# Optimization experiments

Hardware: AMD Instinct MI355X
Metric: run time of the kernel (lower is better)

The kernel has to match this reference:

```python
import jax, jax.numpy as jnp
import numpy as np

B, N1, N2, D, H, L, ITERS = 256, 64, 64, 256, 8, 18, 200
DH = D // H
LAYER_NAMES = ['self', 'cross'] * 9
OFFSET_MULT, NORMAL_MULT = 0.5, 10.0
FLIP = np.array([1.0, -1.0, -1.0], dtype=np.float32)


def setup_inputs() -> dict:
    key = jax.random.key(0)
    ks = jax.random.split(key, 16)
    s = 0.02
    inp = {
        'planeApp1': jax.random.normal(ks[0], (B, N1, D), jnp.float32),
        'planeApp2': jax.random.normal(ks[1], (B, N2, D), jnp.float32),
        'matcher_inputCam': jax.random.normal(ks[2], (B, 7), jnp.float32),
        'parameters1_local': jax.random.normal(ks[3], (B, N1, 3), jnp.float32),
        'parameters2_local': jax.random.normal(ks[4], (B, N2, 3), jnp.float32),
        'app_W': jax.random.normal(ks[5], (D, D), jnp.float32) * s,
        'app_b': jnp.zeros((D,), jnp.float32),
        'desc_W': jax.random.normal(ks[6], (D, D), jnp.float32) * s,
        'desc_b': jnp.zeros((D,), jnp.float32),
        'bin_score': jnp.asarray(1.0, jnp.float32),
        'gnn_Wq': jax.random.normal(ks[7], (L, D, D), jnp.float32) * s,
        'gnn_Wk': jax.random.normal(ks[8], (L, D, D), jnp.float32) * s,
        'gnn_Wv': jax.random.normal(ks[9], (L, D, D), jnp.float32) * s,
        'gnn_Wm': jax.random.normal(ks[10], (L, D, D), jnp.float32) * s,
        'gnn_W1': jax.random.normal(ks[11], (L, 2 * D, 2 * D), jnp.float32) * s,
        'gnn_W2': jax.random.normal(ks[12], (L, 2 * D, D), jnp.float32) * s,
        'gnn_ln1_g': jnp.ones((L, D), jnp.float32),
        'gnn_ln1_b': jnp.zeros((L, D), jnp.float32),
        'gnn_ln2_g': jnp.ones((L, D), jnp.float32),
        'gnn_ln2_b': jnp.zeros((L, D), jnp.float32),
    }
    return inp


def _layer_norm(x, g, b):
    m = jnp.mean(x, -1, keepdims=True)
    v = jnp.var(x, -1, keepdims=True)
    return (x - m) * jax.lax.rsqrt(v + 1e-5) * g + b


def _normalize(x):
    return x / jnp.clip(jnp.linalg.norm(x, axis=-1, keepdims=True), 1e-12)


def _quat_to_rot(q):
    q = q / jnp.linalg.norm(q, axis=-1, keepdims=True)
    w, x, y, z = q[:, 0], q[:, 1], q[:, 2], q[:, 3]
    R = jnp.stack([1 - 2 * (y * y + z * z), 2 * (x * y - w * z), 2 * (x * z + w * y),
                   2 * (x * y + w * z), 1 - 2 * (x * x + z * z), 2 * (y * z - w * x),
                   2 * (x * z - w * y), 2 * (y * z + w * x), 1 - 2 * (x * x + y * y)], axis=-1)
    return R.reshape(-1, 3, 3)


def _warp(plane, quat, tran):
    # plane [B,n,3], quat [B,4], tran [B,3] -> warped plane params [B,n,3]
    R = _quat_to_rot(quat)
    end = jnp.einsum('bij,bnj->bni', R, plane * FLIP) + tran[:, None, :]
    b = end - tran[:, None, :]
    scale = jnp.sum(end * b, -1) / (jnp.linalg.norm(b, axis=-1) + 1e-5) ** 2
    return scale[..., None] * b


def _lin_attn(q, k, v):
    # LoFTR linear attention; q [B,N,H,DH], k/v [B,M,H,DH]
    Q = jax.nn.elu(q) + 1.0
    K = jax.nn.elu(k) + 1.0
    v_len = v.shape[1]
    KV = jnp.einsum('bmhd,bmhe->bhde', K, v / v_len)
    Zden = 1.0 / (jnp.einsum('bnhd,bhd->bnh', Q, K.sum(1)) + 1e-6)
    return jnp.einsum('bnhd,bhde,bnh->bnhe', Q, KV, Zden) * v_len


def _enc_layer(x, src, Wq, Wk, Wv, Wm, W1, W2, g1, be1, g2, be2):
    Bx, N, _ = x.shape
    M = src.shape[1]
    q = (x @ Wq).reshape(Bx, N, H, DH)
    k = (src @ Wk).reshape(Bx, M, H, DH)
    v = (src @ Wv).reshape(Bx, M, H, DH)
    msg = _lin_attn(q, k, v).reshape(Bx, N, D)
    msg = _layer_norm(msg @ Wm, g1, be1)
    msg = _layer_norm(jax.nn.relu(jnp.concatenate([x, msg], -1) @ W1) @ W2, g2, be2)
    return x + msg


def reference(planeApp1, planeApp2, matcher_inputCam, parameters1_local, parameters2_local,
              app_W, app_b, desc_W, desc_b, bin_score,
              gnn_Wq, gnn_Wk, gnn_Wv, gnn_Wm, gnn_W1, gnn_W2,
              gnn_ln1_g, gnn_ln1_b, gnn_ln2_g, gnn_ln2_b):
    tran, quat = matcher_inputCam[:, :3], matcher_inputCam[:, 3:]
    # --- geometric priors (detached in the original) ---
    p2w = parameters2_local * FLIP  # warp with pose_n=1, no rot/tran
    offset2 = jnp.linalg.norm(p2w, axis=-1)  # [B,N2]
    normal2 = _normalize(p2w)
    p1_r = _warp(parameters1_local, quat, tran * 0.0)
    normal1_r = _normalize(p1_r)
    normal_dist = jnp.arccos(jnp.clip(jnp.einsum('bnd,bmd->bnm', normal1_r, normal2), -1.0, 1.0)) / np.pi * 180.0
    p1_rt = _warp(parameters1_local, quat, tran)
    offset1 = jnp.linalg.norm(p1_rt, axis=-1)  # [B,N1]
    normal1_rt = _normalize(p1_rt)
    nTn_rt = jnp.einsum('bnd,bmd->bnm', normal1_rt, normal2)
    od = jnp.where(nTn_rt < 0,
                   jnp.abs(offset1[:, :, None] + offset2[:, None, :]),
                   jnp.abs(offset1[:, :, None] - offset2[:, None, :]))
    offset_dist = jax.lax.stop_gradient(jnp.clip(od, 1e-10, 5.0))
    normal_dist = jax.lax.stop_gradient(normal_dist)
    # --- appearance projection (1x1 Conv1d == per-token linear) ---
    x0 = planeApp1 @ app_W + app_b
    x1 = planeApp2 @ app_W + app_b
    for i, name in enumerate(LAYER_NAMES):
        p = (gnn_Wq[i], gnn_Wk[i], gnn_Wv[i], gnn_Wm[i], gnn_W1[i], gnn_W2[i],
             gnn_ln1_g[i], gnn_ln1_b[i], gnn_ln2_g[i], gnn_ln2_b[i])
        if name == 'self':
            x0, x1 = _enc_layer(x0, x0, *p), _enc_layer(x1, x1, *p)
        else:
            x0, x1 = _enc_layer(x0, x1, *p), _enc_layer(x1, x0, *p)
    d1 = x0 @ desc_W + desc_b
    d2 = x1 @ desc_W + desc_b
    scores = jnp.einsum('bnd,bmd->bnm', d1, d2) / jnp.sqrt(jnp.float32(D))
    scores = scores - offset_dist / OFFSET_MULT - normal_dist / NORMAL_MULT
    # --- padded optimal transport (all rows/cols valid -> no -inf masking) ---
    pc = jnp.broadcast_to(bin_score, (B, N1, 1))
    pr = jnp.broadcast_to(bin_score, (B, 1, N2 + 1))
    Z = jnp.concatenate([jnp.concatenate([scores, pc], axis=2), pr], axis=1)  # [B,N1+1,N2+1]
    norm = -jnp.log(jnp.float32(N1 + N2))
    log_mu = jnp.broadcast_to(jnp.concatenate([jnp.full((N1,), norm), (jnp.log(jnp.float32(N2)) + norm)[None]]), (B, N1 + 1))
    log_nu = jnp.broadcast_to(jnp.concatenate([jnp.full((N2,), norm), (jnp.log(jnp.float32(N1)) + norm)[None]]), (B, N2 + 1))

    def step(carry, _):
        u, v = carry
        u = log_mu - jax.nn.logsumexp(Z + v[:, None, :], axis=2)
        v = log_nu - jax.nn.logsumexp(Z + u[:, :, None], axis=1)
        return (u, v), None

    (u, v), _ = jax.lax.scan(step, (jnp.zeros_like(log_mu), jnp.zeros_like(log_nu)), None, length=ITERS)
    return Z + u[:, :, None] + v[:, None, :] - norm
```

## Files before the change

kernel.cpp:

```cpp
#include <hip/hip_runtime.h>
#include <math.h>
#include <stddef.h>
#include <stdint.h>

typedef unsigned short u16;
typedef unsigned int   u32;

static constexpr int B_   = 256;
static constexpr int N_   = 64;
static constexpr int D_   = 256;
static constexpr int L_   = 18;
static constexpr int RM   = B_ * N_;
static constexpr int RM2  = 2 * RM;
static constexpr size_t SZb = (size_t)RM2 * D_;

typedef __attribute__((ext_vector_type(8))) short bf16x8;
typedef __attribute__((ext_vector_type(4))) float f32x4;

__device__ __forceinline__ float b2f(u16 u) {
    return __uint_as_float(((u32)u) << 16);
}
__device__ __forceinline__ u16 f2b(float f) {
    u32 x = __float_as_uint(f);
    return (u16)((x + 0x7FFFu + ((x >> 16) & 1u)) >> 16);
}
__device__ __forceinline__ void gl_lds16(const void* g, void* l) {
    __builtin_amdgcn_global_load_lds(
        (const __attribute__((address_space(1))) u32*)g,
        (__attribute__((address_space(3))) u32*)l, 16, 0, 0);
}

template<int K, int CONCAT, int RELU, int BIAS, int OUTF, int OUTB>
__global__ __launch_bounds__(256)
void mgemm(const u16* __restrict__ A1, const u16* __restrict__ A2,
           const u16* __restrict__ Bt, const float* __restrict__ bias,
           float* __restrict__ Cf, u16* __restrict__ Cb,
           int M, int splitn)
{
    constexpr int NT = K / 64;
    __shared__ u16 As[2][128 * 64];
    __shared__ u16 Bs[2][128 * 64];
    const int tid  = threadIdx.x;
    const int w    = tid >> 6;
    const int lane = tid & 63;
    const int wr   = w >> 1, wc = w & 1;
    const int row0 = blockIdx.x * 128;
    const int col0 = blockIdx.y * 128;
    const int lr   = lane & 15;
    const int lk   = (lane >> 4) * 8;
    const int srow = lane >> 3;
    const int schk = (lane & 7) * 8;

    auto stage = [&](int t, int buf) {
        const int k0 = t * 64;
        const u16* Aeff; int kloc, lda;
        if (CONCAT) {
            if (k0 < 256) { Aeff = A1; kloc = k0; } else { Aeff = A2; kloc = k0 - 256; }
            lda = 256;
        } else { Aeff = A1; kloc = k0; lda = K; }
        #pragma unroll
        for (int q = 0; q < 4; ++q) {
            const int i = w * 4 + q;
            gl_lds16(Aeff + (size_t)(row0 + i * 8 + srow) * lda + kloc + schk,
                     &As[buf][i * 512]);
            gl_lds16(Bt + (size_t)(col0 + i * 8 + srow) * K + t * 64 + schk,
                     &Bs[buf][i * 512]);
        }
    };

    f32x4 acc[4][4];
    #pragma unroll
    for (int m = 0; m < 4; ++m)
        #pragma unroll
        for (int n = 0; n < 4; ++n)
            acc[m][n] = (f32x4){0.f, 0.f, 0.f, 0.f};

    stage(0, 0);
    __syncthreads();
    #pragma unroll
    for (int t = 0; t < NT; ++t) {
        const int cur = t & 1;
        if (t + 1 < NT) stage(t + 1, cur ^ 1);
        #pragma unroll
        for (int kk = 0; kk < 2; ++kk) {
            bf16x8 af[4], bfr[4];
            #pragma unroll
            for (int m = 0; m < 4; ++m)
                af[m] = *(const bf16x8*)&As[cur][(wr * 64 + m * 16 + lr) * 64 + kk * 32 + lk];
            #pragma unroll
            for (int n = 0; n < 4; ++n)
                bfr[n] = *(const bf16x8*)&Bs[cur][(wc * 64 + n * 16 + lr) * 64 + kk * 32 + lk];
            #pragma unroll
            for (int m = 0; m < 4; ++m)
                #pragma unroll
                for (int n = 0; n < 4; ++n)
                    acc[m][n] = __builtin_amdgcn_mfma_f32_16x16x32_bf16(
                        af[m], bfr[n], acc[m][n], 0, 0, 0);
        }
        __syncthreads();
    }

    const size_t cbase = (size_t)(col0 / splitn) * (size_t)M * splitn;
    const int lc0 = col0 % splitn;
    #pragma unroll
    for (int m = 0; m < 4; ++m) {
        #pragma unroll
        for (int n = 0; n < 4; ++n) {
            const int gc = lc0 + wc * 64 + n * 16 + (lane & 15);
            #pragma unroll
            for (int r = 0; r < 4; ++r) {
                const int gr = row0 + wr * 64 + m * 16 + (lane >> 4) * 4 + r;
                float v = acc[m][n][r];
                if (BIAS) v += bias[gc];
                if (RELU) v = fmaxf(v, 0.f);
                const size_t idx = cbase + (size_t)gr * splitn + gc;
                if (OUTF) Cf[idx] = v;
                if (OUTB) Cb[idx] = f2b(v);
            }
        }
    }
}

template<int K, int RES>
__global__ __launch_bounds__(512)
void mgemm_ln(const u16* __restrict__ A, const u16* __restrict__ Bt,
              const float* __restrict__ g, const float* __restrict__ beta,
              const u16* __restrict__ resb, u16* __restrict__ outb)
{
    constexpr int NT = K / 64;
    __shared__ u16 As[2][128 * 64];
    __shared__ u16 Bs[2][256 * 64];
    __shared__ float rs[4][128], rq[4][128];
    const int tid  = threadIdx.x;
    const int w    = tid >> 6;
    const int lane = tid & 63;
    const int wr   = w >> 2, wc = w & 3;
    const int row0 = blockIdx.x * 128;
    const int lr   = lane & 15;
    const int lk   = (lane >> 4) * 8;
    const int srow = lane >> 3;
    const int schk = (lane & 7) * 8;

    auto stage = [&](int t, int buf) {
        #pragma unroll
        for (int q = 0; q < 2; ++q) {
            const int i = w * 2 + q;
            gl_lds16(A + (size_t)(row0 + i * 8 + srow) * K + t * 64 + schk,
                     &As[buf][i * 512]);
        }
        #pragma unroll
        for (int q = 0; q < 4; ++q) {
            const int i = w * 4 + q;
            gl_lds16(Bt + (size_t)(i * 8 + srow) * K + t * 64 + schk,
                     &Bs[buf][i * 512]);
        }
    };

    f32x4 acc[4][4];
    #pragma unroll
    for (int m = 0; m < 4; ++m)
        #pragma unroll
        for (int n = 0; n < 4; ++n)
            acc[m][n] = (f32x4){0.f, 0.f, 0.f, 0.f};

    stage(0, 0);
    __syncthreads();
    #pragma unroll
    for (int t = 0; t < NT; ++t) {
        const int cur = t & 1;
        if (t + 1 < NT) stage(t + 1, cur ^ 1);
        #pragma unroll
        for (int kk = 0; kk < 2; ++kk) {
            bf16x8 af[4], bfr[4];
            #pragma unroll
            for (int m = 0; m < 4; ++m)
                af[m] = *(const bf16x8*)&As[cur][(wr * 64 + m * 16 + lr) * 64 + kk * 32 + lk];
            #pragma unroll
            for (int n = 0; n < 4; ++n)
                bfr[n] = *(const bf16x8*)&Bs[cur][(wc * 64 + n * 16 + lr) * 64 + kk * 32 + lk];
            #pragma unroll
            for (int m = 0; m < 4; ++m)
                #pragma unroll
                for (int n = 0; n < 4; ++n)
                    acc[m][n] = __builtin_amdgcn_mfma_f32_16x16x32_bf16(
                        af[m], bfr[n], acc[m][n], 0, 0, 0);
        }
        __syncthreads();
    }

    #pragma unroll
    for (int m = 0; m < 4; ++m) {
        #pragma unroll
        for (int r = 0; r < 4; ++r) {
            float s  = acc[m][0][r] + acc[m][1][r] + acc[m][2][r] + acc[m][3][r];
            float s2 = acc[m][0][r]*acc[m][0][r] + acc[m][1][r]*acc[m][1][r]
                     + acc[m][2][r]*acc[m][2][r] + acc[m][3][r]*acc[m][3][r];
            #pragma unroll
            for (int o = 1; o < 16; o <<= 1) {
                s  += __shfl_xor(s,  o);
                s2 += __shfl_xor(s2, o);
            }
            if ((lane & 15) == 0) {
                const int row = wr * 64 + m * 16 + (lane >> 4) * 4 + r;
                rs[wc][row] = s; rq[wc][row] = s2;
            }
        }
    }
    __syncthreads();
    if (tid < 128) {
        const float s = rs[0][tid] + rs[1][tid] + rs[2][tid] + rs[3][tid];
        const float q = rq[0][tid] + rq[1][tid] + rq[2][tid] + rq[3][tid];
        const float mean = s * (1.f / 256.f);
        const float var  = q * (1.f / 256.f) - mean * mean;
        rs[0][tid] = mean;
        rq[0][tid] = rsqrtf(var + 1e-5f);
    }
    __syncthreads();

    float gc[4], bc[4];
    #pragma unroll
    for (int n = 0; n < 4; ++n) {
        const int col = wc * 64 + n * 16 + lr;
        gc[n] = g[col]; bc[n] = beta[col];
    }
    #pragma unroll
    for (int m = 0; m < 4; ++m) {
        #pragma unroll
        for (int r = 0; r < 4; ++r) {
            const int row  = wr * 64 + m * 16 + (lane >> 4) * 4 + r;
            const float mean = rs[0][row], inv = rq[0][row];
            const int gr = row0 + row;
            #pragma unroll
            for (int n = 0; n < 4; ++n) {
                const int col = wc * 64 + n * 16 + lr;
                const size_t idx = (size_t)gr * 256 + col;
                float y = (acc[m][n][r] - mean) * inv * gc[n] + bc[n];
                if (RES) y += b2f(resb[idx]);
                outb[idx] = f2b(y);
            }
        }
    }
}

__global__ __launch_bounds__(256)
void wtrans_kernel(const float* __restrict__ W, u16* __restrict__ Wt,
                   int K, int N, size_t in_lstride, size_t out_lstride,
                   int row_off, int ldk)
{
    __shared__ float T[64][65];
    const int k0 = blockIdx.x * 64, n0 = blockIdx.y * 64, l = blockIdx.z;
    const int t = threadIdx.x;
    const int r = t >> 2, c0 = (t & 3) * 16;
    const float* src = W + (size_t)l * in_lstride;
    #pragma unroll
    for (int q = 0; q < 4; ++q) {
        float4 v = *(const float4*)&src[(size_t)(k0 + r) * N + n0 + c0 + q * 4];
        T[r][c0 + q * 4 + 0] = v.x; T[r][c0 + q * 4 + 1] = v.y;
        T[r][c0 + q * 4 + 2] = v.z; T[r][c0 + q * 4 + 3] = v.w;
    }
    __syncthreads();
    u16 tmp[16];
    #pragma unroll
    for (int i = 0; i < 16; ++i) tmp[i] = f2b(T[c0 + i][r]);
    u16* dst = Wt + (size_t)l * out_lstride + (size_t)(row_off + n0 + r) * ldk + k0 + c0;
    *(uint4*)&dst[0] = *(const uint4*)&tmp[0];
    *(uint4*)&dst[8] = *(const uint4*)&tmp[8];
}

__global__ __launch_bounds__(256)
void cvt2_kernel(const float* __restrict__ s1, const float* __restrict__ s2,
                 u16* __restrict__ dst, int n4half)
{
    int i = blockIdx.x * 256 + threadIdx.x;
    if (i >= 2 * n4half) return;
    const float* s = (i < n4half) ? s1 : s2;
    const int ii = (i < n4half) ? i : i - n4half;
    float4 v = *(const float4*)&s[(size_t)ii * 4];
    u16 o[4] = {f2b(v.x), f2b(v.y), f2b(v.z), f2b(v.w)};
    *(uint2*)&dst[(size_t)i * 4] = *(const uint2*)&o[0];
}

__global__ __launch_bounds__(256)
void attn_kernel(const u16* __restrict__ Q, const u16* __restrict__ K,
                 const u16* __restrict__ V, u16* __restrict__ Mout, int selfl)
{
    const int bid = blockIdx.x;
    const int h = bid & 7;
    const int b = (bid >> 3) & 255;
    const int s = bid >> 11;
    const int ss = selfl ? s : (1 - s);
    const size_t qoff = ((size_t)(s  * RM) + b * N_) * D_ + h * 32;
    const size_t koff = ((size_t)(ss * RM) + b * N_) * D_ + h * 32;

    __shared__ float Ks[64][32];
    __shared__ float Vs[64][32];
    __shared__ float Qs[64][33];
    __shared__ float KV[32][32];
    __shared__ float Ksum[32];
    __shared__ float zden[64];

    const int t = threadIdx.x;
    {
        const int m = t >> 2, d0 = (t & 3) * 8;
        uint4 kq = *(const uint4*)&K[koff + (size_t)m * D_ + d0];
        uint4 vq = *(const uint4*)&V[koff + (size_t)m * D_ + d0];
        uint4 qq = *(const uint4*)&Q[qoff + (size_t)m * D_ + d0];
        const u16* kp = (const u16*)&kq;
        const u16* vp = (const u16*)&vq;
        const u16* qp = (const u16*)&qq;
        #pragma unroll
        for (int j = 0; j < 8; ++j) {
            float kx = b2f(kp[j]);
            Ks[m][d0 + j] = kx > 0.f ? kx + 1.f : __expf(kx);
            Vs[m][d0 + j] = b2f(vp[j]);
            float qx = b2f(qp[j]);
            Qs[m][d0 + j] = qx > 0.f ? qx + 1.f : __expf(qx);
        }
    }
    __syncthreads();
    if (t < 32) {
        float sacc = 0.f;
        for (int m = 0; m < 64; ++m) sacc += Ks[m][t];
        Ksum[t] = sacc;
    }
    for (int i = t; i < 32 * 32; i += 256) {
        const int d = i >> 5, e = i & 31;
        float acc = 0.f;
        for (int m = 0; m < 64; ++m) acc += Ks[m][d] * Vs[m][e];
        KV[d][e] = acc * (1.f / 64.f);
    }
    __syncthreads();
    if (t < 64) {
        float acc = 0.f;
        for (int d = 0; d < 32; ++d) acc += Qs[t][d] * Ksum[d];
        zden[t] = 1.f / (acc + 1e-6f);
    }
    __syncthreads();
    const int n = t >> 2, eg = t & 3;
    float acc[8] = {0.f,0.f,0.f,0.f,0.f,0.f,0.f,0.f};
    for (int d = 0; d < 32; ++d) {
        const float qv = Qs[n][d];
        #pragma unroll
        for (int j = 0; j < 8; ++j) acc[j] += qv * KV[d][eg * 8 + j];
    }
    const float zm = zden[n] * 64.f;
    u16 o[8];
    #pragma unroll
    for (int j = 0; j < 8; ++j) o[j] = f2b(acc[j] * zm);
    *(uint4*)&Mout[qoff + (size_t)n * D_ + eg * 8] = *(const uint4*)&o[0];
}

__global__ __launch_bounds__(64)
void geom_kernel(const float* __restrict__ cam, const float* __restrict__ p1,
                 const float* __restrict__ p2, float* __restrict__ pen)
{
    const int b = blockIdx.x;
    const int n = threadIdx.x;

    const float tx = cam[b*7+0], ty = cam[b*7+1], tz = cam[b*7+2];
    float qw = cam[b*7+3], qx = cam[b*7+4], qy = cam[b*7+5], qz = cam[b*7+6];
    const float qn = rsqrtf(qw*qw + qx*qx + qy*qy + qz*qz);
    qw *= qn; qx *= qn; qy *= qn; qz *= qn;
    const float r00 = 1.f - 2.f*(qy*qy + qz*qz), r01 = 2.f*(qx*qy - qw*qz), r02 = 2.f*(qx*qz + qw*qy);
    const float r10 = 2.f*(qx*qy + qw*qz), r11 = 1.f - 2.f*(qx*qx + qz*qz), r12 = 2.f*(qy*qz - qw*qx);
    const float r20 = 2.f*(qx*qz - qw*qy), r21 = 2.f*(qy*qz + qw*qx), r22 = 1.f - 2.f*(qx*qx + qy*qy);

    const float px =  p1[((size_t)b*64 + n)*3 + 0];
    const float py = -p1[((size_t)b*64 + n)*3 + 1];
    const float pz = -p1[((size_t)b*64 + n)*3 + 2];
    const float ex = r00*px + r01*py + r02*pz;
    const float ey = r10*px + r11*py + r12*pz;
    const float ez = r20*px + r21*py + r22*pz;
    const float el2 = ex*ex + ey*ey + ez*ez;
    const float el  = sqrtf(el2);
    float den = el + 1e-5f; den = den * den;
    const float sr  = el2 / den;
    const float prx = sr*ex, pry = sr*ey, prz = sr*ez;
    const float prl = fmaxf(sqrtf(prx*prx + pry*pry + prz*prz), 1e-12f);
    const float n1rx = prx/prl, n1ry = pry/prl, n1rz = prz/prl;
    const float dot_eb = (ex+tx)*ex + (ey+ty)*ey + (ez+tz)*ez;
    const float st  = dot_eb / den;
    const float ptx = st*ex, pty = st*ey, ptz = st*ez;
    const float o1  = sqrtf(ptx*ptx + pty*pty + ptz*ptz);
    const float ptl = fmaxf(o1, 1e-12f);
    const float n1tx = ptx/ptl, n1ty = pty/ptl, n1tz = ptz/ptl;
    const float ux =  p2[((size_t)b*64 + n)*3 + 0];
    const float uy = -p2[((size_t)b*64 + n)*3 + 1];
    const float uz = -p2[((size_t)b*64 + n)*3 + 2];
    const float o2 = sqrtf(ux*ux + uy*uy + uz*uz);
    const float ul = fmaxf(o2, 1e-12f);

    __shared__ float S[64][4];
    S[n][0] = ux/ul; S[n][1] = uy/ul; S[n][2] = uz/ul; S[n][3] = o2;
    __syncthreads();

    const float RAD2DEG = 57.295779513082323f;
    for (int m = 0; m < 64; ++m) {
        const float nx = S[m][0], ny = S[m][1], nz = S[m][2], o2m = S[m][3];
        float cosr = n1rx*nx + n1ry*ny + n1rz*nz;
        cosr = fminf(fmaxf(cosr, -1.f), 1.f);
        const float ndist = acosf(cosr) * RAD2DEG;
        const float cost = n1tx*nx + n1ty*ny + n1tz*nz;
        float od = (cost < 0.f) ? fabsf(o1 + o2m) : fabsf(o1 - o2m);
        od = fminf(fmaxf(od, 1e-10f), 5.f);
        pen[((size_t)b*64 + n)*64 + m] = od * 2.f + ndist * 0.1f;
    }
}

__global__ __launch_bounds__(256)
void zbuild_kernel(const float* __restrict__ dfeat, const float* __restrict__ pen,
                   const float* __restrict__ binp, float* __restrict__ Z)
{
    const int b = blockIdx.x;
    const float* d1 = dfeat + (size_t)(b * 64) * 256;
    const float* d2 = dfeat + (size_t)(RM + b * 64) * 256;
    __shared__ float D1[64][65], D2[64][65];
    const int tid = threadIdx.x;
    const int txx = tid & 15, tyy = tid >> 4;
    float acc[4][4] = {{0.f,0.f,0.f,0.f},{0.f,0.f,0.f,0.f},
                       {0.f,0.f,0.f,0.f},{0.f,0.f,0.f,0.f}};
    for (int c0 = 0; c0 < 256; c0 += 64) {
        __syncthreads();
        for (int i = tid; i < 64 * 64; i += 256) {
            const int r = i >> 6, c = i & 63;
            D1[r][c] = d1[(size_t)r * 256 + c0 + c];
            D2[r][c] = d2[(size_t)r * 256 + c0 + c];
        }
        __syncthreads();
        for (int c = 0; c < 64; ++c) {
            const float a0 = D1[tyy*4+0][c], a1 = D1[tyy*4+1][c];
            const float a2 = D1[tyy*4+2][c], a3 = D1[tyy*4+3][c];
            const float b0 = D2[txx*4+0][c], b1 = D2[txx*4+1][c];
            const float b2 = D2[txx*4+2][c], b3 = D2[txx*4+3][c];
            acc[0][0] += a0*b0; acc[0][1] += a0*b1; acc[0][2] += a0*b2; acc[0][3] += a0*b3;
            acc[1][0] += a1*b0; acc[1][1] += a1*b1; acc[1][2] += a1*b2; acc[1][3] += a1*b3;
            acc[2][0] += a2*b0; acc[2][1] += a2*b1; acc[2][2] += a2*b2; acc[2][3] += a2*b3;
            acc[3][0] += a3*b0; acc[3][1] += a3*b1; acc[3][2] += a3*b2; acc[3][3] += a3*b3;
        }
    }
    const float bin = *binp;
    #pragma unroll
    for (int i = 0; i < 4; ++i)
        #pragma unroll
        for (int j = 0; j < 4; ++j) {
            const int n = tyy*4 + i, m = txx*4 + j;
            Z[(size_t)b*4225 + n*65 + m] =
                acc[i][j] * (1.f/16.f) - pen[((size_t)b*64 + n)*64 + m];
        }
    if (tid < 65) Z[(size_t)b*4225 + 64*65 + tid] = bin;
    if (tid < 64) Z[(size_t)b*4225 + tid*65 + 64] = bin;
}

__global__ __launch_bounds__(576)
void sinkhorn_kernel(const float* __restrict__ Zin, float* __restrict__ out)
{
    const int b = blockIdx.x;
    __shared__ float uu[72], vv[72];
    const int t  = threadIdx.x;
    const int rr = t >> 3, l8 = t & 7;
    const int act = (rr < 65);
    const float LOG2E = 1.4426950408889634f;
    const float LN2   = 0.69314718055994531f;

    float zrow[9], zcol[9];
    #pragma unroll
    for (int p = 0; p < 9; ++p) {
        const int j = l8 + p * 8;
        const int ok = act && (j < 65);
        zrow[p] = ok ? Zin[(size_t)b * 4225 + rr * 65 + j] * LOG2E : -3.0e38f;
        zcol[p] = ok ? Zin[(size_t)b * 4225 + j * 65 + rr] * LOG2E : -3.0e38f;
    }
    float mr = zrow[0], mc = zcol[0];
    #pragma unroll
    for (int p = 1; p < 9; ++p) { mr = fmaxf(mr, zrow[p]); mc = fmaxf(mc, zcol[p]); }
    #pragma unroll
    for (int o = 1; o < 8; o <<= 1) {
        mr = fmaxf(mr, __shfl_xor(mr, o));
        mc = fmaxf(mc, __shfl_xor(mc, o));
    }
    #pragma unroll
    for (int p = 0; p < 9; ++p) { zrow[p] -= mr; zcol[p] -= mc; }

    if (t < 72) { vv[t] = 0.f; uu[t] = 0.f; }
    __syncthreads();

    const float mu2 = (rr < 64) ? -7.0f : -1.0f;

    for (int it = 0; it < 200; ++it) {
        {
            float s0 = exp2f(zrow[0] + vv[l8]);
            float s1 = exp2f(zrow[1] + vv[l8 + 8]);
            float s2 = exp2f(zrow[2] + vv[l8 + 16]);
            float s3 = exp2f(zrow[3] + vv[l8 + 24]);
            s0 += exp2f(zrow[4] + vv[l8 + 32]);
            s1 += exp2f(zrow[5] + vv[l8 + 40]);
            s2 += exp2f(zrow[6] + vv[l8 + 48]);
            s3 += exp2f(zrow[7] + vv[l8 + 56]);
            s0 += exp2f(zrow[8] + vv[l8 + 64]);
            float sum = (s0 + s1) + (s2 + s3);
            #pragma unroll
            for (int o = 1; o < 8; o <<= 1) sum += __shfl_xor(sum, o);
            if (act && l8 == 0) uu[rr] = mu2 - mr - log2f(sum);
        }
        __syncthreads();
        {
            float s0 = exp2f(zcol[0] + uu[l8]);
            float s1 = exp2f(zcol[1] + uu[l8 + 8]);
            float s2 = exp2f(zcol[2] + uu[l8 + 16]);
            float s3 = exp2f(zcol[3] + uu[l8 + 24]);
            s0 += exp2f(zcol[4] + uu[l8 + 32]);
            s1 += exp2f(zcol[5] + uu[l8 + 40]);
            s2 += exp2f(zcol[6] + uu[l8 + 48]);
            s3 += exp2f(zcol[7] + uu[l8 + 56]);
            s0 += exp2f(zcol[8] + uu[l8 + 64]);
            float sum = (s0 + s1) + (s2 + s3);
            #pragma unroll
            for (int o = 1; o < 8; o <<= 1) sum += __shfl_xor(sum, o);
            if (act && l8 == 0) vv[rr] = mu2 - mc - log2f(sum);
        }
        __syncthreads();
    }
    if (act) {
        const float ur = uu[rr];
        #pragma unroll
        for (int p = 0; p < 9; ++p) {
            const int j = l8 + p * 8;
            if (j < 65)
                out[(size_t)b * 4225 + rr * 65 + j] =
                    (zrow[p] + mr + ur + vv[j] + 7.0f) * LN2;
        }
    }
}

extern "C" void kernel_launch(void* const* d_in, const int* in_sizes, int n_in,
                              void* d_out, int out_size, void* d_ws, size_t ws_size,
                              hipStream_t stream)
{
    const float* planeApp1 = (const float*)d_in[0];
    const float* planeApp2 = (const float*)d_in[1];
    const float* cam       = (const float*)d_in[2];
    const float* p1        = (const float*)d_in[3];
    const float* p2        = (const float*)d_in[4];
    const float* app_W     = (const float*)d_in[5];
    const float* app_b     = (const float*)d_in[6];
    const float* desc_W    = (const float*)d_in[7];
    const float* desc_b    = (const float*)d_in[8];
    const float* bin_score = (const float*)d_in[9];
    const float* Wq        = (const float*)d_in[10];
    const float* Wk        = (const float*)d_in[11];
    const float* Wv        = (const float*)d_in[12];
    const float* Wm        = (const float*)d_in[13];
    const float* W1        = (const float*)d_in[14];
    const float* W2        = (const float*)d_in[15];
    const float* ln1g      = (const float*)d_in[16];
    const float* ln1b      = (const float*)d_in[17];
    const float* ln2g      = (const float*)d_in[18];
    const float* ln2b      = (const float*)d_in[19];

    const size_t wq_elems   = (size_t)L_ * 768 * 256;
    const size_t wm_elems   = (size_t)L_ * 256 * 256;
    const size_t w1_elems   = (size_t)L_ * 512 * 512;
    const size_t w2_elems   = (size_t)L_ * 256 * 512;
    const size_t need = 5 * SZb * 2 + (size_t)B_ * 4096 * 4 +
        (wq_elems + wm_elems + w1_elems + w2_elems + 2 * 65536) * 2;
    if (ws_size < need) return;

    u16* Xb = (u16*)d_ws;
    u16* Qb = Xb + SZb;
    u16* Kb = Qb + SZb;
    u16* Vb = Kb + SZb;
    u16* Tb = Vb + SZb;
    float* pen = (float*)(Tb + SZb);
    u16* wqkv = (u16*)(pen + (size_t)B_ * 4096);
    u16* wmt  = wqkv + wq_elems;
    u16* w1t  = wmt + wm_elems;
    u16* w2t  = w1t + w1_elems;
    u16* appt = w2t + w2_elems;
    u16* dsct = appt + 65536;
    float* outp = (float*)d_out;

    wtrans_kernel<<<dim3(4, 4, L_), 256, 0, stream>>>(Wq, wqkv, 256, 256, 65536, 768*256, 0,   256);
    wtrans_kernel<<<dim3(4, 4, L_), 256, 0, stream>>>(Wk, wqkv, 256, 256, 65536, 768*256, 256, 256);
    wtrans_kernel<<<dim3(4, 4, L_), 256, 0, stream>>>(Wv, wqkv, 256, 256, 65536, 768*256, 512, 256);
    wtrans_kernel<<<dim3(4, 4, L_), 256, 0, stream>>>(Wm, wmt,  256, 256, 65536, 65536,   0,   256);
    wtrans_kernel<<<dim3(8, 8, L_), 256, 0, stream>>>(W1, w1t,  512, 512, 262144, 262144, 0,   512);
    wtrans_kernel<<<dim3(8, 4, L_), 256, 0, stream>>>(W2, w2t,  512, 256, 131072, 131072, 0,   512);
    wtrans_kernel<<<dim3(4, 4, 1),  256, 0, stream>>>(app_W,  appt, 256, 256, 65536, 65536, 0, 256);
    wtrans_kernel<<<dim3(4, 4, 1),  256, 0, stream>>>(desc_W, dsct, 256, 256, 65536, 65536, 0, 256);

    cvt2_kernel<<<(2 * (RM * D_ / 4) + 255) / 256, 256, 0, stream>>>(
        planeApp1, planeApp2, Qb, RM * D_ / 4);

    geom_kernel<<<B_, 64, 0, stream>>>(cam, p1, p2, pen);

    mgemm<256,0,0,1,0,1><<<dim3(RM2/128, 2), 256, 0, stream>>>(
        Qb, nullptr, appt, app_b, nullptr, Xb, RM2, 256);

    for (int i = 0; i < L_; ++i) {
        const int selfl = (i % 2 == 0) ? 1 : 0;
        mgemm<256,0,0,0,0,1><<<dim3(RM2/128, 6), 256, 0, stream>>>(
            Xb, nullptr, wqkv + (size_t)i*768*256, nullptr, nullptr, Qb, RM2, 256);
        attn_kernel<<<2 * B_ * 8, 256, 0, stream>>>(Qb, Kb, Vb, Qb, selfl);
        mgemm_ln<256,0><<<RM2/128, 512, 0, stream>>>(
            Qb, wmt + (size_t)i*65536, ln1g + i*256, ln1b + i*256,
            nullptr, Tb);
        mgemm<512,1,1,0,0,1><<<dim3(RM2/128, 4), 256, 0, stream>>>(
            Xb, Tb, w1t + (size_t)i*262144, nullptr, nullptr, Qb, RM2, 512);
        mgemm_ln<512,1><<<RM2/128, 512, 0, stream>>>(
            Qb, w2t + (size_t)i*131072, ln2g + i*256, ln2b + i*256,
            Xb, Xb);
    }

    mgemm<256,0,0,1,1,0><<<dim3(RM2/128, 2), 256, 0, stream>>>(
        Xb, nullptr, dsct, desc_b, (float*)Qb, nullptr, RM2, 256);

    zbuild_kernel<<<B_, 256, 0, stream>>>((float*)Qb, pen, bin_score, (float*)Vb);
    sinkhorn_kernel<<<B_, 576, 0, stream>>>((float*)Vb, outp);
}
```

Measured before the change: 2.998 ms.

## Fuse MLP W1 ReLU W2 and LayerNorm into one kernel

Replaces the two-kernel MLP (W1 GEMM writing the hidden activation to global memory, then a W2 GEMM with LayerNorm and residual) with one kernel per 64-row tile. The 64x512 ReLU hidden tile is kept in swizzled LDS and consumed directly by the second GEMM. The aim is to cut the global round trip of the hidden activation and one launch per layer. In exchange, weights are read straight from global memory without LDS staging, and the large LDS footprint limits occupancy.

```diff
diff --git a/kernel.cpp b/kernel.cpp
--- a/kernel.cpp
+++ b/kernel.cpp
@@ -240,6 +240,158 @@
             }
         }
     }
+}
+
+__global__ __launch_bounds__(512, 4)
+void mlp_kernel(const u16* __restrict__ Xb, const u16* __restrict__ Tb,
+                const u16* __restrict__ W1t, const u16* __restrict__ W2t,
+                const float* __restrict__ g, const float* __restrict__ beta,
+                u16* __restrict__ outb)
+{
+    __shared__ u16 As[2][64 * 64];
+    __shared__ u16 Hs[64 * 512];
+    const int tid  = threadIdx.x;
+    const int w    = tid >> 6;
+    const int lane = tid & 63;
+    const int lr   = lane & 15;
+    const int lk   = (lane >> 4) * 8;
+    const int row0 = blockIdx.x * 64;
+
+    auto stageA = [&](int t, int buf) {
+        const u16* src = (t < 4) ? Xb : Tb;
+        const int kloc = (t & 3) * 64;
+        gl_lds16(src + (size_t)(row0 + 8 * w + (lane >> 3)) * 256 + kloc + (lane & 7) * 8,
+                 &As[buf][512 * w]);
+    };
+
+    f32x4 acc[4][4];
+    #pragma unroll
+    for (int m = 0; m < 4; ++m)
+        #pragma unroll
+        for (int n = 0; n < 4; ++n)
+            acc[m][n] = (f32x4){0.f, 0.f, 0.f, 0.f};
+
+    stageA(0, 0);
+    __syncthreads();
+    #pragma unroll
+    for (int t = 0; t < 8; ++t) {
+        const int cur = t & 1;
+        if (t + 1 < 8) stageA(t + 1, cur ^ 1);
+        #pragma unroll
+        for (int kk = 0; kk < 2; ++kk) {
+            bf16x8 af[4], bfr[4];
+            #pragma unroll
+            for (int m = 0; m < 4; ++m)
+                af[m] = *(const bf16x8*)&As[cur][(m * 16 + lr) * 64 + kk * 32 + lk];
+            #pragma unroll
+            for (int n = 0; n < 4; ++n)
+                bfr[n] = *(const bf16x8*)&W1t[(size_t)(64 * w + 16 * n + lr) * 512
+                                              + t * 64 + kk * 32 + lk];
+            #pragma unroll
+            for (int m = 0; m < 4; ++m)
+                #pragma unroll
+                for (int n = 0; n < 4; ++n)
+                    acc[m][n] = __builtin_amdgcn_mfma_f32_16x16x32_bf16(
+                        af[m], bfr[n], acc[m][n], 0, 0, 0);
+        }
+        __syncthreads();
+    }
+
+    #pragma unroll
+    for (int m = 0; m < 4; ++m)
+        #pragma unroll
+        for (int n = 0; n < 4; ++n)
+            #pragma unroll
+            for (int r = 0; r < 4; ++r) {
+                const int row = m * 16 + (lane >> 4) * 4 + r;
+                const int col = 64 * w + 16 * n + lr;
+                u32 byte = (u32)(row * 512 + col) * 2;
+                byte ^= (u32)(row & 7) << 4;
+                *(u16*)((char*)Hs + byte) = f2b(fmaxf(acc[m][n][r], 0.f));
+            }
+    __syncthreads();
+
+    f32x4 acc2[4][2];
+    #pragma unroll
+    for (int m = 0; m < 4; ++m)
+        #pragma unroll
+        for (int n = 0; n < 2; ++n)
+            acc2[m][n] = (f32x4){0.f, 0.f, 0.f, 0.f};
+
+    #pragma unroll
+    for (int t = 0; t < 16; ++t) {
+        bf16x8 af[4], bfr[2];
+        #pragma unroll
+        for (int m = 0; m < 4; ++m) {
+            const int row = m * 16 + lr;
+            u32 byte = (u32)(row * 512 + t * 32 + lk) * 2;
+            byte ^= (u32)(row & 7) << 4;
+            af[m] = *(const bf16x8*)((const char*)Hs + byte);
+        }
+        #pragma unroll
+        for (int n = 0; n < 2; ++n)
+            bfr[n] = *(const bf16x8*)&W2t[(size_t)(32 * w + 16 * n + lr) * 512
+                                          + t * 32 + lk];
+        #pragma unroll
+        for (int m = 0; m < 4; ++m)
+            #pragma unroll
+            for (int n = 0; n < 2; ++n)
+                acc2[m][n] = __builtin_amdgcn_mfma_f32_16x16x32_bf16(
+                    af[m], bfr[n], acc2[m][n], 0, 0, 0);
+    }
+
+    float* rs = (float*)&As[0][0];
+    float* rq = rs + 512;
+    __syncthreads();
+    #pragma unroll
+    for (int m = 0; m < 4; ++m)
+        #pragma unroll
+        for (int r = 0; r < 4; ++r) {
+            float s  = acc2[m][0][r] + acc2[m][1][r];
+            float s2 = acc2[m][0][r]*acc2[m][0][r] + acc2[m][1][r]*acc2[m][1][r];
+            #pragma unroll
+            for (int o = 1; o < 16; o <<= 1) {
+                s  += __shfl_xor(s,  o);
+                s2 += __shfl_xor(s2, o);
+            }
+            if ((lane & 15) == 0) {
+                const int row = m * 16 + (lane >> 4) * 4 + r;
+                rs[w * 64 + row] = s; rq[w * 64 + row] = s2;
+            }
+        }
+    __syncthreads();
+    if (tid < 64) {
+        float s = 0.f, q = 0.f;
+        #pragma unroll
+        for (int j = 0; j < 8; ++j) { s += rs[j * 64 + tid]; q += rq[j * 64 + tid]; }
+        const float mean = s * (1.f / 256.f);
+        const float var  = q * (1.f / 256.f) - mean * mean;
+        rs[tid] = mean;
+        rq[tid] = rsqrtf(var + 1e-5f);
+    }
+    __syncthreads();
+
+    float gc[2], bc[2];
+    #pragma unroll
+    for (int n = 0; n < 2; ++n) {
+        const int col = 32 * w + 16 * n + lr;
+        gc[n] = g[col]; bc[n] = beta[col];
+    }
+    #pragma unroll
+    for (int m = 0; m < 4; ++m)
+        #pragma unroll
+        for (int r = 0; r < 4; ++r) {
+            const int row = m * 16 + (lane >> 4) * 4 + r;
+            const float mean = rs[row], inv = rq[row];
+            #pragma unroll
+            for (int n = 0; n < 2; ++n) {
+                const int col = 32 * w + 16 * n + lr;
+                const size_t idx = (size_t)(row0 + row) * 256 + col;
+                float y = (acc2[m][n][r] - mean) * inv * gc[n] + bc[n];
+                y += b2f(outb[idx]);
+                outb[idx] = f2b(y);
+            }
+        }
 }
 
 __global__ __launch_bounds__(256)
@@ -604,11 +756,9 @@
         mgemm_ln<256,0><<<RM2/128, 512, 0, stream>>>(
             Qb, wmt + (size_t)i*65536, ln1g + i*256, ln1b + i*256,
             nullptr, Tb);
-        mgemm<512,1,1,0,0,1><<<dim3(RM2/128, 4), 256, 0, stream>>>(
-            Xb, Tb, w1t + (size_t)i*262144, nullptr, nullptr, Qb, RM2, 512);
-        mgemm_ln<512,1><<<RM2/128, 512, 0, stream>>>(
-            Qb, w2t + (size_t)i*131072, ln2g + i*256, ln2b + i*256,
-            Xb, Xb);
+        mlp_kernel<<<RM2/64, 512, 0, stream>>>(
+            Xb, Tb, w1t + (size_t)i*262144, w2t + (size_t)i*131072,
+            ln2g + i*256, ln2b + i*256, Xb);
     }
 
     mgemm<256,0,0,1,1,0><<<dim3(RM2/128, 2), 256, 0, stream>>>(
```

New measurement: 3.156 ms. 1.05x slower.

## Run Sinkhorn with one wavefront per batch, each lane owning a full row and column

Applied to the files above, without the earlier changes.

The Sinkhorn kernel drops from 576 threads per batch (8 lanes per row, combined with shuffle reductions) to a single 64-lane wavefront. Each lane keeps its whole Z row and Z column in registers and reads the shared u/v vectors with float4 LDS loads. The constant bin row and column are handled in closed form, with one wave-wide shuffle reduction per half-step. This removes the per-row shuffle reductions and the multi-wave barriers. In exchange, all 128 exp2 per lane are serialized on one SIMD per CU, register pressure is high, and the float4 global loads at a row stride of 65 are not 16-byte aligned.

```diff
diff --git a/kernel.cpp b/kernel.cpp
--- a/kernel.cpp
+++ b/kernel.cpp
@@ -451,85 +451,96 @@
     if (tid < 64) Z[(size_t)b*4225 + tid*65 + 64] = bin;
 }
 
-__global__ __launch_bounds__(576)
+__global__ __launch_bounds__(64)
 void sinkhorn_kernel(const float* __restrict__ Zin, float* __restrict__ out)
 {
     const int b = blockIdx.x;
-    __shared__ float uu[72], vv[72];
-    const int t  = threadIdx.x;
-    const int rr = t >> 3, l8 = t & 7;
-    const int act = (rr < 65);
+    const int l = threadIdx.x;
+    __shared__ float uuS[68], vvS[68];
     const float LOG2E = 1.4426950408889634f;
     const float LN2   = 0.69314718055994531f;
-
-    float zrow[9], zcol[9];
-    #pragma unroll
-    for (int p = 0; p < 9; ++p) {
-        const int j = l8 + p * 8;
-        const int ok = act && (j < 65);
-        zrow[p] = ok ? Zin[(size_t)b * 4225 + rr * 65 + j] * LOG2E : -3.0e38f;
-        zcol[p] = ok ? Zin[(size_t)b * 4225 + j * 65 + rr] * LOG2E : -3.0e38f;
-    }
-    float mr = zrow[0], mc = zcol[0];
-    #pragma unroll
-    for (int p = 1; p < 9; ++p) { mr = fmaxf(mr, zrow[p]); mc = fmaxf(mc, zcol[p]); }
-    #pragma unroll
-    for (int o = 1; o < 8; o <<= 1) {
-        mr = fmaxf(mr, __shfl_xor(mr, o));
-        mc = fmaxf(mc, __shfl_xor(mc, o));
-    }
-    #pragma unroll
-    for (int p = 0; p < 9; ++p) { zrow[p] -= mr; zcol[p] -= mc; }
-
-    if (t < 72) { vv[t] = 0.f; uu[t] = 0.f; }
-    __syncthreads();
-
-    const float mu2 = (rr < 64) ? -7.0f : -1.0f;
-
+    const float* Zb = Zin + (size_t)b * 4225;
+
+    float zr[64], zc[64];
+    #pragma unroll
+    for (int q = 0; q < 16; ++q) {
+        float4 v = *(const float4*)&Zb[l * 65 + q * 4];
+        zr[q*4+0] = v.x * LOG2E; zr[q*4+1] = v.y * LOG2E;
+        zr[q*4+2] = v.z * LOG2E; zr[q*4+3] = v.w * LOG2E;
+    }
+    #pragma unroll
+    for (int j = 0; j < 64; ++j)
+        zc[j] = Zb[j * 65 + l] * LOG2E;
+    const float bin2 = Zb[64 * 65] * LOG2E;
+
+    float mr = bin2, mc = bin2;
+    #pragma unroll
+    for (int j = 0; j < 64; ++j) { mr = fmaxf(mr, zr[j]); mc = fmaxf(mc, zc[j]); }
+    #pragma unroll
+    for (int j = 0; j < 64; ++j) { zr[j] -= mr; zc[j] -= mc; }
+    const float zbr = bin2 - mr;
+    const float zbc = bin2 - mc;
+
+    vvS[l] = 0.f;
+    if (l == 0) vvS[64] = 0.f;
+    __syncthreads();
+
+    float uu_l = 0.f, u64 = 0.f;
     for (int it = 0; it < 200; ++it) {
         {
-            float s0 = exp2f(zrow[0] + vv[l8]);
-            float s1 = exp2f(zrow[1] + vv[l8 + 8]);
-            float s2 = exp2f(zrow[2] + vv[l8 + 16]);
-            float s3 = exp2f(zrow[3] + vv[l8 + 24]);
-            s0 += exp2f(zrow[4] + vv[l8 + 32]);
-            s1 += exp2f(zrow[5] + vv[l8 + 40]);
-            s2 += exp2f(zrow[6] + vv[l8 + 48]);
-            s3 += exp2f(zrow[7] + vv[l8 + 56]);
-            s0 += exp2f(zrow[8] + vv[l8 + 64]);
-            float sum = (s0 + s1) + (s2 + s3);
-            #pragma unroll
-            for (int o = 1; o < 8; o <<= 1) sum += __shfl_xor(sum, o);
-            if (act && l8 == 0) uu[rr] = mu2 - mr - log2f(sum);
+            float s0 = 0.f, s1 = 0.f, s2 = 0.f, s3 = 0.f;
+            #pragma unroll
+            for (int q = 0; q < 16; ++q) {
+                float4 v = *(const float4*)&vvS[q * 4];
+                s0 += exp2f(zr[q*4+0] + v.x);
+                s1 += exp2f(zr[q*4+1] + v.y);
+                s2 += exp2f(zr[q*4+2] + v.z);
+                s3 += exp2f(zr[q*4+3] + v.w);
+            }
+            const float vown = vvS[l];
+            const float v64  = vvS[64];
+            const float S = (s0 + s1) + (s2 + s3) + exp2f(zbr + v64);
+            uu_l = -7.f - mr - log2f(S);
+            float t = exp2f(vown);
+            #pragma unroll
+            for (int o = 1; o < 64; o <<= 1) t += __shfl_xor(t, o);
+            u64 = -1.f - bin2 - log2f(t + exp2f(v64));
+            uuS[l] = uu_l;
+            if (l == 0) uuS[64] = u64;
         }
         __syncthreads();
         {
-            float s0 = exp2f(zcol[0] + uu[l8]);
-            float s1 = exp2f(zcol[1] + uu[l8 + 8]);
-            float s2 = exp2f(zcol[2] + uu[l8 + 16]);
-            float s3 = exp2f(zcol[3] + uu[l8 + 24]);
-            s0 += exp2f(zcol[4] + uu[l8 + 32]);
-            s1 += exp2f(zcol[5] + uu[l8 + 40]);
-            s2 += exp2f(zcol[6] + uu[l8 + 48]);
-            s3 += exp2f(zcol[7] + uu[l8 + 56]);
-            s0 += exp2f(zcol[8] + uu[l8 + 64]);
-            float sum = (s0 + s1) + (s2 + s3);
-            #pragma unroll
-            for (int o = 1; o < 8; o <<= 1) sum += __shfl_xor(sum, o);
-            if (act && l8 == 0) vv[rr] = mu2 - mc - log2f(sum);
+            float s0 = 0.f, s1 = 0.f, s2 = 0.f, s3 = 0.f;
+            #pragma unroll
+            for (int q = 0; q < 16; ++q) {
+                float4 u = *(const float4*)&uuS[q * 4];
+                s0 += exp2f(zc[q*4+0] + u.x);
+                s1 += exp2f(zc[q*4+1] + u.y);
+                s2 += exp2f(zc[q*4+2] + u.z);
+                s3 += exp2f(zc[q*4+3] + u.w);
+            }
+            const float uown = uuS[l];
+            const float u64r = uuS[64];
+            const float S = (s0 + s1) + (s2 + s3) + exp2f(zbc + u64r);
+            const float vv_l = -7.f - mc - log2f(S);
+            float t = exp2f(uown);
+            #pragma unroll
+            for (int o = 1; o < 64; o <<= 1) t += __shfl_xor(t, o);
+            const float v64n = -1.f - bin2 - log2f(t + exp2f(u64r));
+            vvS[l] = vv_l;
+            if (l == 0) vvS[64] = v64n;
         }
         __syncthreads();
     }
-    if (act) {
-        const float ur = uu[rr];
-        #pragma unroll
-        for (int p = 0; p < 9; ++p) {
-            const int j = l8 + p * 8;
-            if (j < 65)
-                out[(size_t)b * 4225 + rr * 65 + j] =
-                    (zrow[p] + mr + ur + vv[j] + 7.0f) * LN2;
-        }
-    }
+
+    const float v64 = vvS[64];
+    float* ob = out + (size_t)b * 4225;
+    #pragma unroll
+    for (int j = 0; j < 64; ++j)
+        ob[l * 65 + j] = (zr[j] + mr + uu_l + vvS[j] + 7.f) * LN2;
+    ob[l * 65 + 64] = (bin2 + uu_l + v64 + 7.f) * LN2;
+    ob[64 * 65 + l] = (bin2 + u64 + vvS[l] + 7.f) * LN2;
+    if (l == 0) ob[64 * 65 + 64] = (bin2 + u64 + v64 + 7.f) * LN2;
 }
 
 extern "C" void kernel_launch(void* const* d_in, const int* in_sizes, int n_in,
@@ -615,5 +626,5 @@
         Xb, nullptr, dsct, desc_b, (float*)Qb, nullptr, RM2, 256);
 
     zbuild_kernel<<<B_, 256, 0, stream>>>((float*)Qb, pen, bin_score, (float*)Vb);
-    sinkhorn_kernel<<<B_, 576, 0, stream>>>((float*)Vb, outp);
-}
+    sinkhorn_kernel<<<B_, 64, 0, stream>>>((float*)Vb, outp);
+}
```

Result: slower. 3.309 ms (+10.4%).
